# Kernel tuning notes

Measured on AMD Instinct MI355X. Metric: run time of the kernel, lower is better.

## Reference

```python
import jax, jax.numpy as jnp
import numpy as np

R, S, C, HID = 8192, 128, 32, 64   # rays, samples/ray, grid_chn, mlp_hidden_chn
G = 128                            # voxel grid resolution
COLOR_CHN = 3
NUM_HARM = 3
OPACITY_INIT_BIAS = -5.0
GAIN = 1.0
HE_DIM = 3 * 2 * NUM_HARM + 3      # harmonic embedding dim = 21

def _relu(x):
    return jnp.maximum(x, 0.0)

def _trilinear(grid, p):
    # grid: [G, G, G, Cg] indexed [z, y, x]; p: [N, 3] xyz coords in [-1, 1]
    g = grid.shape[0]
    c = (p + 1.0) * 0.5 * (g - 1)  # align_corners=True convention
    c0f = jnp.floor(c)
    fr = c - c0f
    c0 = jnp.clip(c0f.astype(jnp.int32), 0, g - 1)
    c1 = jnp.clip(c0 + 1, 0, g - 1)
    x0, y0, z0 = c0[:, 0], c0[:, 1], c0[:, 2]
    x1, y1, z1 = c1[:, 0], c1[:, 1], c1[:, 2]
    fx, fy, fz = fr[:, 0:1], fr[:, 1:2], fr[:, 2:3]
    out = jnp.zeros((p.shape[0], grid.shape[-1]), grid.dtype)
    for xi, wx in ((x0, 1.0 - fx), (x1, fx)):
        for yi, wy in ((y0, 1.0 - fy), (y1, fy)):
            for zi, wz in ((z0, 1.0 - fz), (z1, fz)):
                out = out + (wx * wy * wz) * grid[zi, yi, xi]
    return out

def _harmonic(d):
    # [sin(2^i d), cos(2^i d)] for i<NUM_HARM, with raw direction appended
    freqs = 2.0 ** jnp.arange(NUM_HARM, dtype=jnp.float32)
    ang = d[:, None, :] * freqs[None, :, None]  # [R, NH, 3]
    n = d.shape[0]
    return jnp.concatenate([jnp.sin(ang).reshape(n, -1), jnp.cos(ang).reshape(n, -1), d], axis=-1)

def _forward(origins, directions, near, far, feature_grid, Wr, br, Wt1, bt1, Wt2, bt2, Wo1, bo1, Wo2, bo2, Wc1, bc1, Wc2, bc2):
    n_rays = origins.shape[0]
    # stratified midpoints between near and far
    t = near[:, None] + (far - near)[:, None] * (jnp.arange(S, dtype=jnp.float32) + 0.5) / S
    pts = origins[:, None, :] + t[..., None] * directions[:, None, :]  # [R, S, 3]
    feats = _trilinear(feature_grid, pts.reshape(-1, 3)).reshape(n_rays, S, -1)
    # trunk MLP
    e = _relu(feats @ Wt1 + bt1)
    e = _relu(e @ Wt2 + bt2)
    # opacity MLP (last-layer bias carries opacity_init_bias)
    raw = _relu(e @ Wo1 + bo1) @ Wo2 + bo2  # [R, S, 1]
    density = jax.nn.softplus(GAIN * raw[..., 0])
    delta = ((far - near) / S)[:, None]
    alpha = 1.0 - jnp.exp(-delta * density)  # [R, S]
    trans = jnp.cumprod(1.0 - alpha, axis=1)
    T = jnp.concatenate([jnp.ones((n_rays, 1), alpha.dtype), trans[:, :-1]], axis=1)
    w = T * alpha  # compositing weights
    # color branch: harmonic ray-direction encoding added to color-MLP input
    ray_enc = _harmonic(directions) @ Wr + br  # [R, HID]
    cin = e + ray_enc[:, None, :]
    col = jax.nn.sigmoid(_relu(cin @ Wc1 + bc1) @ Wc2 + bc2)  # [R, S, COLOR_CHN]
    color = jnp.einsum('rs,rsc->rc', w, col)
    mask = 1.0 - trans[:, -1]
    color = color + (1.0 - mask)[:, None] * 0.0  # bg_color = 0.0
    return color, mask

def setup_inputs():
    key = jax.random.key(0)
    ks = jax.random.split(key, 16)
    directions = jax.random.normal(ks[0], (R, 3), jnp.float32)
    directions = directions / jnp.linalg.norm(directions, axis=-1, keepdims=True)
    origins = jnp.zeros((R, 3), jnp.float32)
    near = jnp.full((R,), 0.1, jnp.float32)
    far = jnp.full((R,), 1.0, jnp.float32)
    feature_grid = jax.random.normal(ks[1], (G, G, G, C), jnp.float32) * 0.1
    def lin(k, i, o):
        s = (2.0 / (i + o)) ** 0.5
        return jax.random.normal(k, (i, o), jnp.float32) * s
    return {
        'origins': origins, 'directions': directions, 'near': near, 'far': far,
        'feature_grid': feature_grid,
        'Wr': lin(ks[2], HE_DIM, HID), 'br': jnp.zeros((HID,), jnp.float32),
        'Wt1': lin(ks[3], C, HID), 'bt1': jnp.zeros((HID,), jnp.float32),
        'Wt2': lin(ks[4], HID, HID), 'bt2': jnp.zeros((HID,), jnp.float32),
        'Wo1': lin(ks[5], HID, HID), 'bo1': jnp.zeros((HID,), jnp.float32),
        'Wo2': lin(ks[6], HID, 1), 'bo2': jnp.full((1,), OPACITY_INIT_BIAS, jnp.float32),
        'Wc1': lin(ks[7], HID, HID), 'bc1': jnp.zeros((HID,), jnp.float32),
        'Wc2': lin(ks[8], HID, COLOR_CHN), 'bc2': jnp.zeros((COLOR_CHN,), jnp.float32),
    }

def reference(origins, directions, near, far, feature_grid, Wr, br, Wt1, bt1, Wt2, bt2, Wo1, bo1, Wo2, bo2, Wc1, bc1, Wc2, bc2):
    return _forward(origins, directions, near, far, feature_grid, Wr, br, Wt1, bt1, Wt2, bt2, Wo1, bo1, Wo2, bo2, Wc1, bc1, Wc2, bc2)
```

## Files before the change

kernel.cpp:

```cpp
#include <hip/hip_runtime.h>
#include <math.h>

#define NRAYS 8192
#define XPAD 72

#define WS_PERM_BYTE 28672

typedef short s16x8 __attribute__((ext_vector_type(8)));
typedef float f32x4 __attribute__((ext_vector_type(4)));

__device__ __forceinline__ unsigned short f2bf(float x){
  unsigned u = __float_as_uint(x);
  u += 0x7FFF + ((u >> 16) & 1);
  return (unsigned short)(u >> 16);
}
__device__ __forceinline__ float bf2f(unsigned short s){ return __uint_as_float(((unsigned)s) << 16); }
__device__ __forceinline__ float softplusf_(float x){ return (x > 20.f) ? x : log1pf(expf(x)); }
__device__ __forceinline__ float sigmoidf_(float x){ return 1.f / (1.f + expf(-x)); }

__global__ void prep_weights(const float* __restrict__ Wt1, const float* __restrict__ Wt2,
                             const float* __restrict__ Wo1, const float* __restrict__ Wc1,
                             unsigned short* __restrict__ ws)
{
  const int i0 = blockIdx.x * blockDim.x + threadIdx.x;
  const int st = gridDim.x * blockDim.x;
  for (int i = i0; i < 2048; i += st){ int n = i >> 5, k = i & 31; ws[i]         = f2bf(Wt1[k * 64 + n]); }
  for (int i = i0; i < 4096; i += st){ int n = i >> 6, k = i & 63; ws[2048 + i]  = f2bf(Wt2[k * 64 + n]); }
  for (int i = i0; i < 4096; i += st){ int n = i >> 6, k = i & 63; ws[6144 + i]  = f2bf(Wo1[k * 64 + n]); }
  for (int i = i0; i < 4096; i += st){ int n = i >> 6, k = i & 63; ws[10240 + i] = f2bf(Wc1[k * 64 + n]); }
}

__global__ __launch_bounds__(1024) void sort_rays(const float* __restrict__ dirs,
                                                  int* __restrict__ perm)
{
  __shared__ int h[64];
  __shared__ unsigned char keys[NRAYS];
  const int tid = threadIdx.x;
  if (tid < 64) h[tid] = 0;
  __syncthreads();
  for (int r = tid; r < NRAYS; r += 1024){
    const float dx = dirs[3*r], dy = dirs[3*r+1], dz = dirs[3*r+2];
    const int qx = min(3, max(0, (int)((dx + 1.f) * 2.f)));
    const int qy = min(3, max(0, (int)((dy + 1.f) * 2.f)));
    const int qz = min(3, max(0, (int)((dz + 1.f) * 2.f)));
    const int k = (qx << 4) | (qy << 2) | qz;
    keys[r] = (unsigned char)k;
    atomicAdd(&h[k], 1);
  }
  __syncthreads();
  if (tid == 0){ int s = 0; for (int i = 0; i < 64; ++i){ int c = h[i]; h[i] = s; s += c; } }
  __syncthreads();
  for (int r = tid; r < NRAYS; r += 1024){
    const int pos = atomicAdd(&h[keys[r]], 1);
    perm[pos] = r;
  }
}

__device__ __forceinline__ void layer64(const s16x8 a[4][2], const unsigned short* __restrict__ wt,
                                        const float* __restrict__ bias, int ln15, int quad,
                                        f32x4 acc[4][4])
{
  float bv[4];
#pragma unroll
  for (int nt = 0; nt < 4; ++nt) bv[nt] = bias[nt * 16 + ln15];
#pragma unroll
  for (int mt = 0; mt < 4; ++mt)
#pragma unroll
    for (int nt = 0; nt < 4; ++nt){ f32x4 c; c[0] = bv[nt]; c[1] = bv[nt]; c[2] = bv[nt]; c[3] = bv[nt]; acc[mt][nt] = c; }
#pragma unroll
  for (int ks = 0; ks < 2; ++ks){
    s16x8 b[4];
#pragma unroll
    for (int nt = 0; nt < 4; ++nt)
      b[nt] = *(const s16x8*)(wt + (nt * 16 + ln15) * 64 + ks * 32 + quad * 8);
#pragma unroll
    for (int mt = 0; mt < 4; ++mt)
#pragma unroll
      for (int nt = 0; nt < 4; ++nt)
        acc[mt][nt] = __builtin_amdgcn_mfma_f32_16x16x32_bf16(a[mt][ks], b[nt], acc[mt][nt], 0, 0, 0);
  }
}

__device__ __forceinline__ void store_relu(unsigned short* __restrict__ sX, int wrow, int ln15, int quad,
                                           const f32x4 acc[4][4])
{
#pragma unroll
  for (int mt = 0; mt < 4; ++mt){
    const int rowb = wrow + mt * 16 + quad * 4;
#pragma unroll
    for (int nt = 0; nt < 4; ++nt){
      const int col = nt * 16 + ln15;
#pragma unroll
      for (int r = 0; r < 4; ++r)
        sX[(rowb + r) * XPAD + col] = f2bf(fmaxf(acc[mt][nt][r], 0.f));
    }
  }
}

extern "C" __global__ __launch_bounds__(256, 4)
void lightplane_fwd(const float* __restrict__ origins, const float* __restrict__ dirs,
                    const float* __restrict__ nearv,   const float* __restrict__ farv,
                    const float* __restrict__ grid,
                    const float* __restrict__ Wr,  const float* __restrict__ br,
                    const float* __restrict__ bt1, const float* __restrict__ bt2,
                    const float* __restrict__ bo1,
                    const float* __restrict__ Wo2, const float* __restrict__ bo2,
                    const float* __restrict__ bc1,
                    const float* __restrict__ Wc2, const float* __restrict__ bc2,
                    const unsigned short* __restrict__ ws,
                    const int* __restrict__ perm,
                    float* __restrict__ out)
{
  __shared__ unsigned short s_X[256 * XPAD];
  __shared__ float s_enc[2][64];
  __shared__ float s_part[2][2][4];
  __shared__ float s_wtot[4];

  const int tid   = threadIdx.x;
  const int lane  = tid & 63;
  const int wv    = tid >> 6;
  const int ln15  = lane & 15, quad = lane >> 4;
  const int wrow  = wv * 64;
  const int r_loc = tid >> 7;
  const int s_idx = tid & 127;

  const int bid = (int)blockIdx.x;
  const int wg  = (bid & 7) * ((int)gridDim.x >> 3) + (bid >> 3);
  const int ray = perm[wg * 2 + r_loc];

  const float dx = dirs[ray * 3 + 0], dy = dirs[ray * 3 + 1], dz = dirs[ray * 3 + 2];
  const float ox = origins[ray * 3 + 0], oy = origins[ray * 3 + 1], oz = origins[ray * 3 + 2];
  const float nr = nearv[ray], fa = farv[ray];
  const float t  = nr + (fa - nr) * ((s_idx + 0.5f) * (1.0f / 128.0f));
  const float px = fmaf(t, dx, ox), py = fmaf(t, dy, oy), pz = fmaf(t, dz, oz);

  const float cx = (px + 1.f) * 63.5f, cy = (py + 1.f) * 63.5f, cz = (pz + 1.f) * 63.5f;
  const float fx0 = floorf(cx), fy0 = floorf(cy), fz0 = floorf(cz);
  const float frx = cx - fx0, fry = cy - fy0, frz = cz - fz0;
  int ix0 = min(max((int)fx0, 0), 127), iy0 = min(max((int)fy0, 0), 127), iz0 = min(max((int)fz0, 0), 127);
  int ix1 = min(ix0 + 1, 127), iy1 = min(iy0 + 1, 127), iz1 = min(iz0 + 1, 127);
  const float wxs[2] = {1.f - frx, frx}, wys[2] = {1.f - fry, fry}, wzs[2] = {1.f - frz, frz};
  const int xi[2] = {ix0, ix1}, yi[2] = {iy0, iy1}, zi[2] = {iz0, iz1};

  float fe[32];
#pragma unroll
  for (int k = 0; k < 32; ++k) fe[k] = 0.f;

  const float4* __restrict__ gb = (const float4*)grid;
#pragma unroll
  for (int zz = 0; zz < 2; ++zz)
#pragma unroll
    for (int yy = 0; yy < 2; ++yy) {
      const size_t rowb = (size_t)((zi[zz] * 128 + yi[yy]) * 128) * 8;
      const float4* p0 = gb + rowb + (size_t)xi[0] * 8;
      const float4* p1 = gb + rowb + (size_t)xi[1] * 8;
      float4 v0[8], v1[8];
#pragma unroll
      for (int q = 0; q < 8; ++q) { v0[q] = p0[q]; v1[q] = p1[q]; }
      const float wzy = wzs[zz] * wys[yy];
      const float wA = wzy * wxs[0], wB = wzy * wxs[1];
#pragma unroll
      for (int q = 0; q < 8; ++q) {
        fe[q * 4 + 0] = fmaf(wA, v0[q].x, fmaf(wB, v1[q].x, fe[q * 4 + 0]));
        fe[q * 4 + 1] = fmaf(wA, v0[q].y, fmaf(wB, v1[q].y, fe[q * 4 + 1]));
        fe[q * 4 + 2] = fmaf(wA, v0[q].z, fmaf(wB, v1[q].z, fe[q * 4 + 2]));
        fe[q * 4 + 3] = fmaf(wA, v0[q].w, fmaf(wB, v1[q].w, fe[q * 4 + 3]));
      }
    }

#pragma unroll
  for (int q = 0; q < 4; ++q) {
    s16x8 v;
#pragma unroll
    for (int j = 0; j < 8; ++j) v[j] = (short)f2bf(fe[q * 8 + j]);
    *(s16x8*)&s_X[tid * XPAD + q * 8] = v;
  }

  if (tid < 128) {
    const int rr = tid >> 6, j = tid & 63;
    const int rg = perm[wg * 2 + rr];
    const float ddx = dirs[rg * 3 + 0], ddy = dirs[rg * 3 + 1], ddz = dirs[rg * 3 + 2];
    float h[21]; float f = 1.f;
#pragma unroll
    for (int q = 0; q < 3; ++q) {
      h[q * 3 + 0] = sinf(ddx * f); h[q * 3 + 1] = sinf(ddy * f); h[q * 3 + 2] = sinf(ddz * f);
      h[9 + q * 3 + 0] = cosf(ddx * f); h[9 + q * 3 + 1] = cosf(ddy * f); h[9 + q * 3 + 2] = cosf(ddz * f);
      f *= 2.f;
    }
    h[18] = ddx; h[19] = ddy; h[20] = ddz;
    float a = br[j];
#pragma unroll
    for (int i = 0; i < 21; ++i) a = fmaf(h[i], Wr[i * 64 + j], a);
    s_enc[rr][j] = a;
  }

  f32x4 acc[4][4];

  {
    s16x8 a1[4];
#pragma unroll
    for (int mt = 0; mt < 4; ++mt)
      a1[mt] = *(const s16x8*)&s_X[(wrow + mt * 16 + ln15) * XPAD + quad * 8];
    float bv[4];
#pragma unroll
    for (int nt = 0; nt < 4; ++nt) bv[nt] = bt1[nt * 16 + ln15];
#pragma unroll
    for (int mt = 0; mt < 4; ++mt)
#pragma unroll
      for (int nt = 0; nt < 4; ++nt){ f32x4 c; c[0]=bv[nt];c[1]=bv[nt];c[2]=bv[nt];c[3]=bv[nt]; acc[mt][nt]=c; }
    s16x8 b[4];
#pragma unroll
    for (int nt = 0; nt < 4; ++nt)
      b[nt] = *(const s16x8*)(ws + (nt * 16 + ln15) * 32 + quad * 8);
#pragma unroll
    for (int mt = 0; mt < 4; ++mt)
#pragma unroll
      for (int nt = 0; nt < 4; ++nt)
        acc[mt][nt] = __builtin_amdgcn_mfma_f32_16x16x32_bf16(a1[mt], b[nt], acc[mt][nt], 0, 0, 0);
    store_relu(s_X, wrow, ln15, quad, acc);
  }

  {
    s16x8 a[4][2];
#pragma unroll
    for (int ks = 0; ks < 2; ++ks)
#pragma unroll
      for (int mt = 0; mt < 4; ++mt)
        a[mt][ks] = *(const s16x8*)&s_X[(wrow + mt * 16 + ln15) * XPAD + ks * 32 + quad * 8];
    layer64(a, ws + 2048, bt2, ln15, quad, acc);
    store_relu(s_X, wrow, ln15, quad, acc);
  }

  s16x8 ea[4][2];
#pragma unroll
  for (int ks = 0; ks < 2; ++ks)
#pragma unroll
    for (int mt = 0; mt < 4; ++mt)
      ea[mt][ks] = *(const s16x8*)&s_X[(wrow + mt * 16 + ln15) * XPAD + ks * 32 + quad * 8];

  layer64(ea, ws + 6144, bo1, ln15, quad, acc);
  store_relu(s_X, wrow, ln15, quad, acc);
  float raw = bo2[0];
#pragma unroll
  for (int q = 0; q < 8; ++q) {
    s16x8 v = *(const s16x8*)&s_X[tid * XPAD + q * 8];
#pragma unroll
    for (int j = 0; j < 8; ++j)
      raw = fmaf(bf2f((unsigned short)v[j]), Wo2[q * 8 + j], raw);
  }
  const float density = softplusf_(raw);
  const float delta   = (fa - nr) * (1.0f / 128.0f);
  const float alpha   = 1.f - expf(-delta * density);

  __syncthreads();

  {
    s16x8 a[4][2];
#pragma unroll
    for (int ks = 0; ks < 2; ++ks) {
      const float* ep = &s_enc[r_loc][ks * 32 + quad * 8];
      float4 e0 = *(const float4*)ep;
      float4 e1 = *(const float4*)(ep + 4);
      float encv[8] = {e0.x, e0.y, e0.z, e0.w, e1.x, e1.y, e1.z, e1.w};
#pragma unroll
      for (int mt = 0; mt < 4; ++mt) {
        s16x8 v;
#pragma unroll
        for (int j = 0; j < 8; ++j)
          v[j] = (short)f2bf(bf2f((unsigned short)ea[mt][ks][j]) + encv[j]);
        a[mt][ks] = v;
      }
    }
    layer64(a, ws + 10240, bc1, ln15, quad, acc);
    store_relu(s_X, wrow, ln15, quad, acc);
  }
  float c0 = bc2[0], c1 = bc2[1], c2 = bc2[2];
#pragma unroll
  for (int q = 0; q < 8; ++q) {
    s16x8 v = *(const s16x8*)&s_X[tid * XPAD + q * 8];
#pragma unroll
    for (int j = 0; j < 8; ++j) {
      const float h = bf2f((unsigned short)v[j]);
      c0 = fmaf(h, Wc2[(q * 8 + j) * 3 + 0], c0);
      c1 = fmaf(h, Wc2[(q * 8 + j) * 3 + 1], c1);
      c2 = fmaf(h, Wc2[(q * 8 + j) * 3 + 2], c2);
    }
  }
  c0 = sigmoidf_(c0); c1 = sigmoidf_(c1); c2 = sigmoidf_(c2);

  float sc = 1.f - alpha;
#pragma unroll
  for (int off = 1; off < 64; off <<= 1) {
    const float u = __shfl_up(sc, off, 64);
    if (lane >= off) sc *= u;
  }
  float excl = __shfl_up(sc, 1, 64);
  if (lane == 0) excl = 1.f;
  if (lane == 63) s_wtot[wv] = sc;
  __syncthreads();
  const int w_in_ray = s_idx >> 6;
  const float prefix = w_in_ray ? s_wtot[r_loc * 2] : 1.f;
  const float wgt = prefix * excl * alpha;

  float p0 = wgt * c0, p1 = wgt * c1, p2 = wgt * c2;
#pragma unroll
  for (int off = 32; off > 0; off >>= 1) {
    p0 += __shfl_down(p0, off, 64);
    p1 += __shfl_down(p1, off, 64);
    p2 += __shfl_down(p2, off, 64);
  }
  if (lane == 0) {
    s_part[r_loc][w_in_ray][0] = p0; s_part[r_loc][w_in_ray][1] = p1; s_part[r_loc][w_in_ray][2] = p2;
  }
  __syncthreads();
  if (s_idx == 0) {
    out[ray * 3 + 0] = s_part[r_loc][0][0] + s_part[r_loc][1][0];
    out[ray * 3 + 1] = s_part[r_loc][0][1] + s_part[r_loc][1][1];
    out[ray * 3 + 2] = s_part[r_loc][0][2] + s_part[r_loc][1][2];
    out[NRAYS * 3 + ray] = 1.f - s_wtot[r_loc * 2] * s_wtot[r_loc * 2 + 1];
  }
}

extern "C" void kernel_launch(void* const* d_in, const int* in_sizes, int n_in,
                              void* d_out, int out_size, void* d_ws, size_t ws_size,
                              hipStream_t stream)
{
  (void)in_sizes; (void)n_in; (void)out_size; (void)ws_size;
  const float* origins = (const float*)d_in[0];
  const float* dirs    = (const float*)d_in[1];
  const float* nearv   = (const float*)d_in[2];
  const float* farv    = (const float*)d_in[3];
  const float* grid    = (const float*)d_in[4];
  const float* Wr  = (const float*)d_in[5];
  const float* br  = (const float*)d_in[6];
  const float* Wt1 = (const float*)d_in[7];
  const float* bt1 = (const float*)d_in[8];
  const float* Wt2 = (const float*)d_in[9];
  const float* bt2 = (const float*)d_in[10];
  const float* Wo1 = (const float*)d_in[11];
  const float* bo1 = (const float*)d_in[12];
  const float* Wo2 = (const float*)d_in[13];
  const float* bo2 = (const float*)d_in[14];
  const float* Wc1 = (const float*)d_in[15];
  const float* bc1 = (const float*)d_in[16];
  const float* Wc2 = (const float*)d_in[17];
  const float* bc2 = (const float*)d_in[18];
  unsigned short* ws = (unsigned short*)d_ws;
  int* perm = (int*)((char*)d_ws + WS_PERM_BYTE);
  float* out = (float*)d_out;

  prep_weights<<<16, 256, 0, stream>>>(Wt1, Wt2, Wo1, Wc1, ws);
  sort_rays<<<1, 1024, 0, stream>>>(dirs, perm);
  lightplane_fwd<<<NRAYS / 2, 256, 0, stream>>>(origins, dirs, nearv, farv, grid,
                                                Wr, br, bt1, bt2, bo1, Wo2, bo2,
                                                bc1, Wc2, bc2, ws, perm, out);
}
```

Before: 553.2 us.

## Drop ray-direction sort and split MLP layers into column halves to cut registers

```diff
diff --git a/kernel.cpp b/kernel.cpp
--- a/kernel.cpp
+++ b/kernel.cpp
@@ -3,8 +3,6 @@
 
 #define NRAYS 8192
 #define XPAD 72
-
-#define WS_PERM_BYTE 28672
 
 typedef short s16x8 __attribute__((ext_vector_type(8)));
 typedef float f32x4 __attribute__((ext_vector_type(4)));
@@ -30,66 +28,40 @@
   for (int i = i0; i < 4096; i += st){ int n = i >> 6, k = i & 63; ws[10240 + i] = f2bf(Wc1[k * 64 + n]); }
 }
 
-__global__ __launch_bounds__(1024) void sort_rays(const float* __restrict__ dirs,
-                                                  int* __restrict__ perm)
-{
-  __shared__ int h[64];
-  __shared__ unsigned char keys[NRAYS];
-  const int tid = threadIdx.x;
-  if (tid < 64) h[tid] = 0;
-  __syncthreads();
-  for (int r = tid; r < NRAYS; r += 1024){
-    const float dx = dirs[3*r], dy = dirs[3*r+1], dz = dirs[3*r+2];
-    const int qx = min(3, max(0, (int)((dx + 1.f) * 2.f)));
-    const int qy = min(3, max(0, (int)((dy + 1.f) * 2.f)));
-    const int qz = min(3, max(0, (int)((dz + 1.f) * 2.f)));
-    const int k = (qx << 4) | (qy << 2) | qz;
-    keys[r] = (unsigned char)k;
-    atomicAdd(&h[k], 1);
-  }
-  __syncthreads();
-  if (tid == 0){ int s = 0; for (int i = 0; i < 64; ++i){ int c = h[i]; h[i] = s; s += c; } }
-  __syncthreads();
-  for (int r = tid; r < NRAYS; r += 1024){
-    const int pos = atomicAdd(&h[keys[r]], 1);
-    perm[pos] = r;
-  }
-}
-
-__device__ __forceinline__ void layer64(const s16x8 a[4][2], const unsigned short* __restrict__ wt,
-                                        const float* __restrict__ bias, int ln15, int quad,
-                                        f32x4 acc[4][4])
-{
-  float bv[4];
-#pragma unroll
-  for (int nt = 0; nt < 4; ++nt) bv[nt] = bias[nt * 16 + ln15];
+__device__ __forceinline__ void layer64_half(const s16x8 a[4][2], const unsigned short* __restrict__ wt,
+                                             const float* __restrict__ bias, int ln15, int quad, int nh,
+                                             f32x4 acc[4][2])
+{
+  float bv[2];
+#pragma unroll
+  for (int nt = 0; nt < 2; ++nt) bv[nt] = bias[nh * 32 + nt * 16 + ln15];
 #pragma unroll
   for (int mt = 0; mt < 4; ++mt)
 #pragma unroll
-    for (int nt = 0; nt < 4; ++nt){ f32x4 c; c[0] = bv[nt]; c[1] = bv[nt]; c[2] = bv[nt]; c[3] = bv[nt]; acc[mt][nt] = c; }
+    for (int nt = 0; nt < 2; ++nt){ f32x4 c; c[0]=bv[nt];c[1]=bv[nt];c[2]=bv[nt];c[3]=bv[nt]; acc[mt][nt]=c; }
 #pragma unroll
   for (int ks = 0; ks < 2; ++ks){
-    s16x8 b[4];
-#pragma unroll
-    for (int nt = 0; nt < 4; ++nt)
-      b[nt] = *(const s16x8*)(wt + (nt * 16 + ln15) * 64 + ks * 32 + quad * 8);
+    s16x8 b[2];
+#pragma unroll
+    for (int nt = 0; nt < 2; ++nt)
+      b[nt] = *(const s16x8*)(wt + (nh * 32 + nt * 16 + ln15) * 64 + ks * 32 + quad * 8);
 #pragma unroll
     for (int mt = 0; mt < 4; ++mt)
 #pragma unroll
-      for (int nt = 0; nt < 4; ++nt)
+      for (int nt = 0; nt < 2; ++nt)
         acc[mt][nt] = __builtin_amdgcn_mfma_f32_16x16x32_bf16(a[mt][ks], b[nt], acc[mt][nt], 0, 0, 0);
   }
 }
 
-__device__ __forceinline__ void store_relu(unsigned short* __restrict__ sX, int wrow, int ln15, int quad,
-                                           const f32x4 acc[4][4])
+__device__ __forceinline__ void store_relu_half(unsigned short* __restrict__ sX, int wrow, int ln15,
+                                                int quad, int nh, const f32x4 acc[4][2])
 {
 #pragma unroll
   for (int mt = 0; mt < 4; ++mt){
     const int rowb = wrow + mt * 16 + quad * 4;
 #pragma unroll
-    for (int nt = 0; nt < 4; ++nt){
-      const int col = nt * 16 + ln15;
+    for (int nt = 0; nt < 2; ++nt){
+      const int col = nh * 32 + nt * 16 + ln15;
 #pragma unroll
       for (int r = 0; r < 4; ++r)
         sX[(rowb + r) * XPAD + col] = f2bf(fmaxf(acc[mt][nt][r], 0.f));
@@ -108,7 +80,6 @@
                     const float* __restrict__ bc1,
                     const float* __restrict__ Wc2, const float* __restrict__ bc2,
                     const unsigned short* __restrict__ ws,
-                    const int* __restrict__ perm,
                     float* __restrict__ out)
 {
   __shared__ unsigned short s_X[256 * XPAD];
@@ -123,10 +94,7 @@
   const int wrow  = wv * 64;
   const int r_loc = tid >> 7;
   const int s_idx = tid & 127;
-
-  const int bid = (int)blockIdx.x;
-  const int wg  = (bid & 7) * ((int)gridDim.x >> 3) + (bid >> 3);
-  const int ray = perm[wg * 2 + r_loc];
+  const int ray   = blockIdx.x * 2 + r_loc;
 
   const float dx = dirs[ray * 3 + 0], dy = dirs[ray * 3 + 1], dz = dirs[ray * 3 + 2];
   const float ox = origins[ray * 3 + 0], oy = origins[ray * 3 + 1], oz = origins[ray * 3 + 2];
@@ -178,7 +146,7 @@
 
   if (tid < 128) {
     const int rr = tid >> 6, j = tid & 63;
-    const int rg = perm[wg * 2 + rr];
+    const int rg = blockIdx.x * 2 + rr;
     const float ddx = dirs[rg * 3 + 0], ddy = dirs[rg * 3 + 1], ddz = dirs[rg * 3 + 2];
     float h[21]; float f = 1.f;
 #pragma unroll
@@ -194,30 +162,33 @@
     s_enc[rr][j] = a;
   }
 
-  f32x4 acc[4][4];
+  f32x4 acc[4][2];
 
   {
     s16x8 a1[4];
 #pragma unroll
     for (int mt = 0; mt < 4; ++mt)
       a1[mt] = *(const s16x8*)&s_X[(wrow + mt * 16 + ln15) * XPAD + quad * 8];
-    float bv[4];
-#pragma unroll
-    for (int nt = 0; nt < 4; ++nt) bv[nt] = bt1[nt * 16 + ln15];
-#pragma unroll
-    for (int mt = 0; mt < 4; ++mt)
-#pragma unroll
-      for (int nt = 0; nt < 4; ++nt){ f32x4 c; c[0]=bv[nt];c[1]=bv[nt];c[2]=bv[nt];c[3]=bv[nt]; acc[mt][nt]=c; }
-    s16x8 b[4];
-#pragma unroll
-    for (int nt = 0; nt < 4; ++nt)
-      b[nt] = *(const s16x8*)(ws + (nt * 16 + ln15) * 32 + quad * 8);
-#pragma unroll
-    for (int mt = 0; mt < 4; ++mt)
-#pragma unroll
-      for (int nt = 0; nt < 4; ++nt)
-        acc[mt][nt] = __builtin_amdgcn_mfma_f32_16x16x32_bf16(a1[mt], b[nt], acc[mt][nt], 0, 0, 0);
-    store_relu(s_X, wrow, ln15, quad, acc);
+#pragma unroll
+    for (int nh = 0; nh < 2; ++nh) {
+      float bv[2];
+#pragma unroll
+      for (int nt = 0; nt < 2; ++nt) bv[nt] = bt1[nh * 32 + nt * 16 + ln15];
+#pragma unroll
+      for (int mt = 0; mt < 4; ++mt)
+#pragma unroll
+        for (int nt = 0; nt < 2; ++nt){ f32x4 c; c[0]=bv[nt];c[1]=bv[nt];c[2]=bv[nt];c[3]=bv[nt]; acc[mt][nt]=c; }
+      s16x8 b[2];
+#pragma unroll
+      for (int nt = 0; nt < 2; ++nt)
+        b[nt] = *(const s16x8*)(ws + (nh * 32 + nt * 16 + ln15) * 32 + quad * 8);
+#pragma unroll
+      for (int mt = 0; mt < 4; ++mt)
+#pragma unroll
+        for (int nt = 0; nt < 2; ++nt)
+          acc[mt][nt] = __builtin_amdgcn_mfma_f32_16x16x32_bf16(a1[mt], b[nt], acc[mt][nt], 0, 0, 0);
+      store_relu_half(s_X, wrow, ln15, quad, nh, acc);
+    }
   }
 
   {
@@ -227,8 +198,11 @@
 #pragma unroll
       for (int mt = 0; mt < 4; ++mt)
         a[mt][ks] = *(const s16x8*)&s_X[(wrow + mt * 16 + ln15) * XPAD + ks * 32 + quad * 8];
-    layer64(a, ws + 2048, bt2, ln15, quad, acc);
-    store_relu(s_X, wrow, ln15, quad, acc);
+#pragma unroll
+    for (int nh = 0; nh < 2; ++nh) {
+      layer64_half(a, ws + 2048, bt2, ln15, quad, nh, acc);
+      store_relu_half(s_X, wrow, ln15, quad, nh, acc);
+    }
   }
 
   s16x8 ea[4][2];
@@ -238,8 +212,11 @@
     for (int mt = 0; mt < 4; ++mt)
       ea[mt][ks] = *(const s16x8*)&s_X[(wrow + mt * 16 + ln15) * XPAD + ks * 32 + quad * 8];
 
-  layer64(ea, ws + 6144, bo1, ln15, quad, acc);
-  store_relu(s_X, wrow, ln15, quad, acc);
+#pragma unroll
+  for (int nh = 0; nh < 2; ++nh) {
+    layer64_half(ea, ws + 6144, bo1, ln15, quad, nh, acc);
+    store_relu_half(s_X, wrow, ln15, quad, nh, acc);
+  }
   float raw = bo2[0];
 #pragma unroll
   for (int q = 0; q < 8; ++q) {
@@ -255,24 +232,43 @@
   __syncthreads();
 
   {
-    s16x8 a[4][2];
+    float encv[2][8];
 #pragma unroll
     for (int ks = 0; ks < 2; ++ks) {
       const float* ep = &s_enc[r_loc][ks * 32 + quad * 8];
       float4 e0 = *(const float4*)ep;
       float4 e1 = *(const float4*)(ep + 4);
-      float encv[8] = {e0.x, e0.y, e0.z, e0.w, e1.x, e1.y, e1.z, e1.w};
-#pragma unroll
-      for (int mt = 0; mt < 4; ++mt) {
-        s16x8 v;
-#pragma unroll
-        for (int j = 0; j < 8; ++j)
-          v[j] = (short)f2bf(bf2f((unsigned short)ea[mt][ks][j]) + encv[j]);
-        a[mt][ks] = v;
+      encv[ks][0]=e0.x; encv[ks][1]=e0.y; encv[ks][2]=e0.z; encv[ks][3]=e0.w;
+      encv[ks][4]=e1.x; encv[ks][5]=e1.y; encv[ks][6]=e1.z; encv[ks][7]=e1.w;
+    }
+#pragma unroll
+    for (int nh = 0; nh < 2; ++nh) {
+      float bv[2];
+#pragma unroll
+      for (int nt = 0; nt < 2; ++nt) bv[nt] = bc1[nh * 32 + nt * 16 + ln15];
+#pragma unroll
+      for (int mt = 0; mt < 4; ++mt)
+#pragma unroll
+        for (int nt = 0; nt < 2; ++nt){ f32x4 c; c[0]=bv[nt];c[1]=bv[nt];c[2]=bv[nt];c[3]=bv[nt]; acc[mt][nt]=c; }
+#pragma unroll
+      for (int ks = 0; ks < 2; ++ks) {
+        s16x8 b[2];
+#pragma unroll
+        for (int nt = 0; nt < 2; ++nt)
+          b[nt] = *(const s16x8*)(ws + 10240 + (nh * 32 + nt * 16 + ln15) * 64 + ks * 32 + quad * 8);
+#pragma unroll
+        for (int mt = 0; mt < 4; ++mt) {
+          s16x8 ca;
+#pragma unroll
+          for (int j = 0; j < 8; ++j)
+            ca[j] = (short)f2bf(bf2f((unsigned short)ea[mt][ks][j]) + encv[ks][j]);
+#pragma unroll
+          for (int nt = 0; nt < 2; ++nt)
+            acc[mt][nt] = __builtin_amdgcn_mfma_f32_16x16x32_bf16(ca, b[nt], acc[mt][nt], 0, 0, 0);
+        }
       }
-    }
-    layer64(a, ws + 10240, bc1, ln15, quad, acc);
-    store_relu(s_X, wrow, ln15, quad, acc);
+      store_relu_half(s_X, wrow, ln15, quad, nh, acc);
+    }
   }
   float c0 = bc2[0], c1 = bc2[1], c2 = bc2[2];
 #pragma unroll
@@ -346,12 +342,10 @@
   const float* Wc2 = (const float*)d_in[17];
   const float* bc2 = (const float*)d_in[18];
   unsigned short* ws = (unsigned short*)d_ws;
-  int* perm = (int*)((char*)d_ws + WS_PERM_BYTE);
   float* out = (float*)d_out;
 
   prep_weights<<<16, 256, 0, stream>>>(Wt1, Wt2, Wo1, Wc1, ws);
-  sort_rays<<<1, 1024, 0, stream>>>(dirs, perm);
   lightplane_fwd<<<NRAYS / 2, 256, 0, stream>>>(origins, dirs, nearv, farv, grid,
                                                 Wr, br, bt1, bt2, bo1, Wo2, bo2,
-                                                bc1, Wc2, bc2, ws, perm, out);
-}
+                                                bc1, Wc2, bc2, ws, out);
+}
```

Measured after the change: 507.4 us. -8.3%, faster.
